# Kernel optimization log

Hardware: AMD Instinct MI355X
Metric: run time of the kernel (lower is better)

Reference implementation:

```python
import jax, jax.numpy as jnp
import numpy as np

EMBED_DIM = 256
NUM_HEADS = 8
HEAD_DIM = EMBED_DIM // NUM_HEADS
ADJ_CHANNELS = 4
B, N = 8, 1024


def setup_inputs() -> dict:
    key = jax.random.key(0)
    ks = jax.random.split(key, 12)
    s = 1.0 / np.sqrt(EMBED_DIM)
    sa = 1.0 / np.sqrt(ADJ_CHANNELS)
    return {
        "x": jax.random.normal(ks[0], (B, N, EMBED_DIM), dtype=jnp.float32),
        "adj": jax.random.uniform(ks[1], (B, N, N, ADJ_CHANNELS), dtype=jnp.float32),
        "Wq": jax.random.uniform(ks[2], (EMBED_DIM, EMBED_DIM), jnp.float32, -s, s),
        "bq": jnp.zeros((EMBED_DIM,), jnp.float32),
        "Wk": jax.random.uniform(ks[3], (EMBED_DIM, EMBED_DIM), jnp.float32, -s, s),
        "bk": jnp.zeros((EMBED_DIM,), jnp.float32),
        "Wv": jax.random.uniform(ks[4], (EMBED_DIM, EMBED_DIM), jnp.float32, -s, s),
        "bv": jnp.zeros((EMBED_DIM,), jnp.float32),
        "Wo": jax.random.uniform(ks[5], (EMBED_DIM, EMBED_DIM), jnp.float32, -s, s),
        "bo": jnp.zeros((EMBED_DIM,), jnp.float32),
        "Wa": jax.random.uniform(ks[6], (ADJ_CHANNELS, NUM_HEADS), jnp.float32, -sa, sa),
        "ba": jnp.zeros((NUM_HEADS,), jnp.float32),
    }


def reference(x, adj, Wq, bq, Wk, bk, Wv, bv, Wo, bo, Wa, ba):
    Bs, Ns, E = x.shape
    H, D = NUM_HEADS, HEAD_DIM
    def heads(W, b):
        return (x @ W + b).reshape(Bs, Ns, H, D).transpose(0, 2, 1, 3)  # [B,H,N,D]
    Q, K, V = heads(Wq, bq), heads(Wk, bk), heads(Wv, bv)
    # adjacency-derived additive bias: [B,N,N,C] -> [B,N,N,H] -> [B,H,N,N]
    bias = jnp.moveaxis(adj @ Wa + ba, -1, 1)
    scores = jnp.einsum("bhnd,bhmd->bhnm", Q, K) / np.sqrt(D) + bias
    attn = jax.nn.softmax(scores, axis=-1)
    ctx = jnp.einsum("bhnm,bhmd->bhnd", attn, V)  # [B,H,N,D]
    ctx = ctx.transpose(0, 2, 1, 3).reshape(Bs, Ns, E)
    return ctx @ Wo + bo + x
```

## Files before the change

kernel.cpp:

```cpp
#include <hip/hip_runtime.h>
#include <hip/hip_bf16.h>

#define BATCH 8
#define SEQ   1024
#define EMB   256
#define NH    8
#define HD    32
#define QSCALE 0.2550030053f

typedef __attribute__((ext_vector_type(8))) short short8;
typedef __attribute__((ext_vector_type(4))) float floatx4;

__device__ __forceinline__ ushort f2bf(float f) {
    __hip_bfloat16 h = __float2bfloat16(f);
    return *reinterpret_cast<ushort*>(&h);
}

__device__ __forceinline__ void gload_lds16(const float4* g, float4* l) {
    __builtin_amdgcn_global_load_lds(
        (const __attribute__((address_space(1))) unsigned int*)g,
        (__attribute__((address_space(3))) unsigned int*)l, 16, 0, 0);
}

__global__ __launch_bounds__(256) void prep_kernel(
    const float* __restrict__ Wq, const float* __restrict__ Wk,
    const float* __restrict__ Wv, const float* __restrict__ Wo,
    ushort* __restrict__ Wqt, ushort* __restrict__ Wkt,
    ushort* __restrict__ Wvt, ushort* __restrict__ Wot)
{
    __shared__ float tilebuf[32][33];
    const int blk = blockIdx.x;
    const int mat = blk >> 6, tile = blk & 63;
    const int ti = tile >> 3, tj = tile & 7;
    const float* W = (mat == 0) ? Wq : (mat == 1) ? Wk : (mat == 2) ? Wv : Wo;
    ushort* Wt = (mat == 0) ? Wqt : (mat == 1) ? Wkt : (mat == 2) ? Wvt : Wot;
    const float scale = (mat == 0) ? QSCALE : 1.0f;

    const int tx = threadIdx.x & 31, ty = threadIdx.x >> 5;
    #pragma unroll
    for (int p = 0; p < 4; ++p)
        tilebuf[ty + p * 8][tx] = W[(size_t)(ti * 32 + ty + p * 8) * EMB + tj * 32 + tx];
    __syncthreads();
    #pragma unroll
    for (int p = 0; p < 4; ++p)
        Wt[(size_t)(tj * 32 + ty + p * 8) * EMB + ti * 32 + tx] =
            f2bf(tilebuf[tx][ty + p * 8] * scale);
}

__global__ __launch_bounds__(256) void qkv_gemm(
    const float* __restrict__ x,
    const ushort* __restrict__ Wqt, const ushort* __restrict__ Wkt,
    const ushort* __restrict__ Wvt,
    const float* __restrict__ bq, const float* __restrict__ bk,
    const float* __restrict__ bv,
    ushort* __restrict__ Qb, ushort* __restrict__ Kb, ushort* __restrict__ Vt)
{
    const int mat = blockIdx.y;
    const ushort* __restrict__ Wt = (mat == 0) ? Wqt : (mat == 1) ? Wkt : Wvt;
    const float* __restrict__ bias = (mat == 0) ? bq : (mat == 1) ? bk : bv;
    const float bscale = (mat == 0) ? QSCALE : 1.0f;

    const int w = threadIdx.x >> 6, lane = threadIdx.x & 63;
    const int quad = lane >> 4, l16 = lane & 15;
    const int row0 = blockIdx.x * 64 + w * 16;

    floatx4 acc[16];
    #pragma unroll
    for (int i = 0; i < 16; ++i) acc[i] = (floatx4){0.f, 0.f, 0.f, 0.f};

    const float* __restrict__ xrow = x + (size_t)(row0 + l16) * EMB + quad * 8;

    #pragma unroll
    for (int ks = 0; ks < 8; ++ks) {
        const float4 xa0 = *(const float4*)(xrow + ks * 32);
        const float4 xa1 = *(const float4*)(xrow + ks * 32 + 4);
        ushort au[8] = {f2bf(xa0.x), f2bf(xa0.y), f2bf(xa0.z), f2bf(xa0.w),
                        f2bf(xa1.x), f2bf(xa1.y), f2bf(xa1.z), f2bf(xa1.w)};
        const short8 a = *(const short8*)au;
        #pragma unroll
        for (int i = 0; i < 16; ++i) {
            const short8 bf = *(const short8*)(Wt + (size_t)(i * 16 + l16) * EMB + ks * 32 + quad * 8);
            acc[i] = __builtin_amdgcn_mfma_f32_16x16x32_bf16(a, bf, acc[i], 0, 0, 0);
        }
    }

    const int gr0 = row0 + quad * 4;
    if (mat < 2) {
        ushort* __restrict__ dst = (mat == 0) ? Qb : Kb;
        #pragma unroll
        for (int i = 0; i < 16; ++i) {
            const int c = i * 16 + l16, h = c >> 5, d = c & (HD - 1);
            const float bb = bias[c] * bscale;
            #pragma unroll
            for (int r = 0; r < 4; ++r) {
                const int gr = gr0 + r, b = gr >> 10, n = gr & (SEQ - 1);
                dst[((size_t)(b * NH + h) * SEQ + n) * HD + d] = f2bf(acc[i][r] + bb);
            }
        }
    } else {
        const int b = gr0 >> 10, n0 = gr0 & (SEQ - 1);
        #pragma unroll
        for (int i = 0; i < 16; ++i) {
            const int c = i * 16 + l16, h = c >> 5, d = c & (HD - 1);
            const float bb = bias[c];
            ushort4 t4;
            t4.x = f2bf(acc[i][0] + bb); t4.y = f2bf(acc[i][1] + bb);
            t4.z = f2bf(acc[i][2] + bb); t4.w = f2bf(acc[i][3] + bb);
            *(ushort4*)(Vt + ((size_t)(b * NH + h) * HD + d) * SEQ + n0) = t4;
        }
    }
}

__global__ __launch_bounds__(512) void attn_kernel(
    const ushort* __restrict__ Qb, const ushort* __restrict__ Kb,
    const ushort* __restrict__ Vt, const float* __restrict__ adj,
    const float* __restrict__ Wa, const float* __restrict__ ba,
    float* __restrict__ cp, float* __restrict__ lsum)
{
    __shared__ float4 Atile[2][16][65];
    __shared__ ushort Plds[NH][2][16][36];
    const int tid = threadIdx.x, h = tid >> 6, lane = tid & 63;
    const int quad = lane >> 4, l16 = lane & 15;
    const int q0 = blockIdx.x * 16, b = blockIdx.y, z = blockIdx.z;
    const int bh = b * NH + h;
    const int kz = z * 512;

    const float LOG2E = 1.4426950408889634f;
    const float wa0 = Wa[0 * NH + h] * LOG2E, wa1 = Wa[1 * NH + h] * LOG2E;
    const float wa2 = Wa[2 * NH + h] * LOG2E, wa3 = Wa[3 * NH + h] * LOG2E;
    const float bah = ba[h] * LOG2E;

    const short8 aq = *(const short8*)(Qb + ((size_t)bh * SEQ + q0 + l16) * HD + quad * 8);

    floatx4 o0 = {0.f, 0.f, 0.f, 0.f}, o1 = {0.f, 0.f, 0.f, 0.f};
    float lrow[4] = {0.f, 0.f, 0.f, 0.f};

    const float4* __restrict__ adjb = (const float4*)adj + (size_t)b * SEQ * SEQ;
    const float4* __restrict__ asrc0 = adjb + (size_t)(q0 + 2 * h)     * SEQ + kz + lane;
    const float4* __restrict__ asrc1 = adjb + (size_t)(q0 + 2 * h + 1) * SEQ + kz + lane;

    const ushort* __restrict__ Kbase = Kb + (size_t)bh * SEQ * HD + (size_t)l16 * HD + quad * 8;
    const ushort* __restrict__ Vb0 = Vt + ((size_t)bh * HD + l16) * SEQ + quad * 8;
    const ushort* __restrict__ Vb1 = Vt + ((size_t)bh * HD + 16 + l16) * SEQ + quad * 8;

    gload_lds16(asrc0, &Atile[0][2 * h][0]);
    gload_lds16(asrc1, &Atile[0][2 * h + 1][0]);
    __syncthreads();

    for (int it = 0; it < 8; ++it) {
        const int cur = it & 1;
        const int key0 = kz + it * 64;

        if (it < 7) {
            gload_lds16(asrc0 + (it + 1) * 64, &Atile[cur ^ 1][2 * h][0]);
            gload_lds16(asrc1 + (it + 1) * 64, &Atile[cur ^ 1][2 * h + 1][0]);
        }

        const short8 k0 = *(const short8*)(Kbase + (size_t)(key0)      * HD);
        const short8 k1 = *(const short8*)(Kbase + (size_t)(key0 + 16) * HD);
        const short8 k2 = *(const short8*)(Kbase + (size_t)(key0 + 32) * HD);
        const short8 k3 = *(const short8*)(Kbase + (size_t)(key0 + 48) * HD);
        const floatx4 zz = {0.f, 0.f, 0.f, 0.f};
        floatx4 s0 = __builtin_amdgcn_mfma_f32_16x16x32_bf16(aq, k0, zz, 0, 0, 0);
        floatx4 s1 = __builtin_amdgcn_mfma_f32_16x16x32_bf16(aq, k1, zz, 0, 0, 0);
        floatx4 s2 = __builtin_amdgcn_mfma_f32_16x16x32_bf16(aq, k2, zz, 0, 0, 0);
        floatx4 s3 = __builtin_amdgcn_mfma_f32_16x16x32_bf16(aq, k3, zz, 0, 0, 0);

        #pragma unroll
        for (int r = 0; r < 4; ++r) {
            const int row = quad * 4 + r;
            const float4 a0 = Atile[cur][row][l16];
            const float4 a1 = Atile[cur][row][16 + l16];
            const float4 a2 = Atile[cur][row][32 + l16];
            const float4 a3 = Atile[cur][row][48 + l16];
            const float b0 = fmaf(a0.x, wa0, fmaf(a0.y, wa1, fmaf(a0.z, wa2, fmaf(a0.w, wa3, bah))));
            const float b1 = fmaf(a1.x, wa0, fmaf(a1.y, wa1, fmaf(a1.z, wa2, fmaf(a1.w, wa3, bah))));
            const float b2 = fmaf(a2.x, wa0, fmaf(a2.y, wa1, fmaf(a2.z, wa2, fmaf(a2.w, wa3, bah))));
            const float b3 = fmaf(a3.x, wa0, fmaf(a3.y, wa1, fmaf(a3.z, wa2, fmaf(a3.w, wa3, bah))));
            const float p0 = exp2f(s0[r] + b0);
            const float p1 = exp2f(s1[r] + b1);
            const float p2 = exp2f(s2[r] + b2);
            const float p3 = exp2f(s3[r] + b3);
            lrow[r] += (p0 + p1) + (p2 + p3);
            Plds[h][0][row][l16]      = f2bf(p0);
            Plds[h][0][row][16 + l16] = f2bf(p1);
            Plds[h][1][row][l16]      = f2bf(p2);
            Plds[h][1][row][16 + l16] = f2bf(p3);
        }
        __builtin_amdgcn_s_waitcnt(0xc07f);

        const short8 ap0 = *(const short8*)&Plds[h][0][l16][quad * 8];
        const short8 ap1 = *(const short8*)&Plds[h][1][l16][quad * 8];
        const short8 v0 = *(const short8*)(Vb0 + key0);
        const short8 v1 = *(const short8*)(Vb1 + key0);
        const short8 v2 = *(const short8*)(Vb0 + key0 + 32);
        const short8 v3 = *(const short8*)(Vb1 + key0 + 32);
        o0 = __builtin_amdgcn_mfma_f32_16x16x32_bf16(ap0, v0, o0, 0, 0, 0);
        o1 = __builtin_amdgcn_mfma_f32_16x16x32_bf16(ap0, v1, o1, 0, 0, 0);
        o0 = __builtin_amdgcn_mfma_f32_16x16x32_bf16(ap1, v2, o0, 0, 0, 0);
        o1 = __builtin_amdgcn_mfma_f32_16x16x32_bf16(ap1, v3, o1, 0, 0, 0);

        __syncthreads();
    }

    #pragma unroll
    for (int r = 0; r < 4; ++r) {
        lrow[r] += __shfl_xor(lrow[r], 1, 64);
        lrow[r] += __shfl_xor(lrow[r], 2, 64);
        lrow[r] += __shfl_xor(lrow[r], 4, 64);
        lrow[r] += __shfl_xor(lrow[r], 8, 64);
    }

    float* __restrict__ cpz = cp + (size_t)z * BATCH * SEQ * EMB;
    float* __restrict__ lsz = lsum + (size_t)z * BATCH * SEQ * NH;
    #pragma unroll
    for (int r = 0; r < 4; ++r) {
        const size_t grow = (size_t)b * SEQ + q0 + quad * 4 + r;
        cpz[grow * EMB + h * HD + l16]      = o0[r];
        cpz[grow * EMB + h * HD + 16 + l16] = o1[r];
        if (l16 == 0) lsz[grow * NH + h] = lrow[r];
    }
}

__global__ __launch_bounds__(256) void outproj_gemm(
    const float* __restrict__ cp, const float* __restrict__ lsum,
    const ushort* __restrict__ Wot, const float* __restrict__ bo,
    const float* __restrict__ x, float* __restrict__ out)
{
    const int w = threadIdx.x >> 6, lane = threadIdx.x & 63;
    const int quad = lane >> 4, l16 = lane & 15;
    const int row0 = blockIdx.x * 64 + w * 16;
    const int arow = row0 + l16;
    const float* __restrict__ cp1 = cp + (size_t)BATCH * SEQ * EMB;
    const float* __restrict__ l1  = lsum + (size_t)BATCH * SEQ * NH;

    floatx4 acc[16];
    #pragma unroll
    for (int i = 0; i < 16; ++i) acc[i] = (floatx4){0.f, 0.f, 0.f, 0.f};

    #pragma unroll
    for (int ks = 0; ks < 8; ++ks) {
        const float invl = 1.0f / (lsum[(size_t)arow * NH + ks] + l1[(size_t)arow * NH + ks]);
        const size_t cb = (size_t)arow * EMB + ks * 32 + quad * 8;
        const float4 c00 = *(const float4*)(cp + cb);
        const float4 c01 = *(const float4*)(cp + cb + 4);
        const float4 c10 = *(const float4*)(cp1 + cb);
        const float4 c11 = *(const float4*)(cp1 + cb + 4);
        ushort au[8] = {
            f2bf((c00.x + c10.x) * invl), f2bf((c00.y + c10.y) * invl),
            f2bf((c00.z + c10.z) * invl), f2bf((c00.w + c10.w) * invl),
            f2bf((c01.x + c11.x) * invl), f2bf((c01.y + c11.y) * invl),
            f2bf((c01.z + c11.z) * invl), f2bf((c01.w + c11.w) * invl)};
        const short8 a = *(const short8*)au;
        #pragma unroll
        for (int i = 0; i < 16; ++i) {
            const short8 bfr = *(const short8*)(Wot + (size_t)(i * 16 + l16) * EMB + ks * 32 + quad * 8);
            acc[i] = __builtin_amdgcn_mfma_f32_16x16x32_bf16(a, bfr, acc[i], 0, 0, 0);
        }
    }

    const int gr0 = row0 + quad * 4;
    #pragma unroll
    for (int i = 0; i < 16; ++i) {
        const int c = i * 16 + l16;
        const float bov = bo[c];
        #pragma unroll
        for (int r = 0; r < 4; ++r) {
            const size_t idx = (size_t)(gr0 + r) * EMB + c;
            out[idx] = acc[i][r] + bov + x[idx];
        }
    }
}

extern "C" void kernel_launch(void* const* d_in, const int* in_sizes, int n_in,
                              void* d_out, int out_size, void* d_ws, size_t ws_size,
                              hipStream_t stream) {
    const float* x   = (const float*)d_in[0];
    const float* adj = (const float*)d_in[1];
    const float* Wq  = (const float*)d_in[2];
    const float* bq  = (const float*)d_in[3];
    const float* Wk  = (const float*)d_in[4];
    const float* bk  = (const float*)d_in[5];
    const float* Wv  = (const float*)d_in[6];
    const float* bv  = (const float*)d_in[7];
    const float* Wo  = (const float*)d_in[8];
    const float* bo  = (const float*)d_in[9];
    const float* Wa  = (const float*)d_in[10];
    const float* ba  = (const float*)d_in[11];

    const size_t per = (size_t)BATCH * NH * SEQ * HD;
    ushort* Qb  = (ushort*)d_ws;
    ushort* Kb  = Qb + per;
    ushort* Vt  = Kb + per;
    ushort* Wqt = Vt + per;
    ushort* Wkt = Wqt + EMB * EMB;
    ushort* Wvt = Wkt + EMB * EMB;
    ushort* Wot = Wvt + EMB * EMB;
    float*  cp  = (float*)(Wot + EMB * EMB);
    float*  ls  = cp + 2 * (size_t)BATCH * SEQ * EMB;

    prep_kernel<<<256, 256, 0, stream>>>(Wq, Wk, Wv, Wo, Wqt, Wkt, Wvt, Wot);
    qkv_gemm<<<dim3(BATCH * SEQ / 64, 3), 256, 0, stream>>>(
        x, Wqt, Wkt, Wvt, bq, bk, bv, Qb, Kb, Vt);
    attn_kernel<<<dim3(SEQ / 16, BATCH, 2), 512, 0, stream>>>(
        Qb, Kb, Vt, adj, Wa, ba, cp, ls);
    outproj_gemm<<<BATCH * SEQ / 64, 256, 0, stream>>>(
        cp, ls, Wot, bo, x, (float*)d_out);
}
```

Measured before the change: 300.6 us.

## Compute transposed scores in attention to pass P via shuffles instead of LDS

The attention kernel now computes S^T (K as the A operand, Q as B), so each lane holds probabilities for one query row across keys. The P tile is packed to bf16 pairs and redistributed with cross-lane shuffles into the B-operand layout for the PV MFMA, removing the per-wave LDS staging buffer and its waitcnt. Row-sum reduction and output stores are adjusted to the transposed layout, and launch bounds gain a minimum-occupancy hint. It adds shuffle instructions and changes the adj LDS read pattern, which could introduce bank conflicts.

```diff
diff --git a/kernel.cpp b/kernel.cpp
--- a/kernel.cpp
+++ b/kernel.cpp
@@ -14,6 +14,9 @@
 __device__ __forceinline__ ushort f2bf(float f) {
     __hip_bfloat16 h = __float2bfloat16(f);
     return *reinterpret_cast<ushort*>(&h);
+}
+__device__ __forceinline__ unsigned int pack2bf(float lo, float hi) {
+    return (unsigned int)f2bf(lo) | ((unsigned int)f2bf(hi) << 16);
 }
 
 __device__ __forceinline__ void gload_lds16(const float4* g, float4* l) {
@@ -111,14 +114,13 @@
     }
 }
 
-__global__ __launch_bounds__(512) void attn_kernel(
+__global__ __launch_bounds__(512, 8) void attn_kernel(
     const ushort* __restrict__ Qb, const ushort* __restrict__ Kb,
     const ushort* __restrict__ Vt, const float* __restrict__ adj,
     const float* __restrict__ Wa, const float* __restrict__ ba,
     float* __restrict__ cp, float* __restrict__ lsum)
 {
     __shared__ float4 Atile[2][16][65];
-    __shared__ ushort Plds[NH][2][16][36];
     const int tid = threadIdx.x, h = tid >> 6, lane = tid & 63;
     const int quad = lane >> 4, l16 = lane & 15;
     const int q0 = blockIdx.x * 16, b = blockIdx.y, z = blockIdx.z;
@@ -133,7 +135,7 @@
     const short8 aq = *(const short8*)(Qb + ((size_t)bh * SEQ + q0 + l16) * HD + quad * 8);
 
     floatx4 o0 = {0.f, 0.f, 0.f, 0.f}, o1 = {0.f, 0.f, 0.f, 0.f};
-    float lrow[4] = {0.f, 0.f, 0.f, 0.f};
+    float lacc = 0.f;
 
     const float4* __restrict__ adjb = (const float4*)adj + (size_t)b * SEQ * SEQ;
     const float4* __restrict__ asrc0 = adjb + (size_t)(q0 + 2 * h)     * SEQ + kz + lane;
@@ -143,83 +145,83 @@
     const ushort* __restrict__ Vb0 = Vt + ((size_t)bh * HD + l16) * SEQ + quad * 8;
     const ushort* __restrict__ Vb1 = Vt + ((size_t)bh * HD + 16 + l16) * SEQ + quad * 8;
 
+    const int laneA = l16 | ((quad & 1) << 5);
+    const int laneB = laneA + 16;
+    const bool lowsel = quad < 2;
+
     gload_lds16(asrc0, &Atile[0][2 * h][0]);
     gload_lds16(asrc1, &Atile[0][2 * h + 1][0]);
     __syncthreads();
 
     for (int it = 0; it < 8; ++it) {
         const int cur = it & 1;
-        const int key0 = kz + it * 64;
-
         if (it < 7) {
             gload_lds16(asrc0 + (it + 1) * 64, &Atile[cur ^ 1][2 * h][0]);
             gload_lds16(asrc1 + (it + 1) * 64, &Atile[cur ^ 1][2 * h + 1][0]);
         }
-
-        const short8 k0 = *(const short8*)(Kbase + (size_t)(key0)      * HD);
-        const short8 k1 = *(const short8*)(Kbase + (size_t)(key0 + 16) * HD);
-        const short8 k2 = *(const short8*)(Kbase + (size_t)(key0 + 32) * HD);
-        const short8 k3 = *(const short8*)(Kbase + (size_t)(key0 + 48) * HD);
-        const floatx4 zz = {0.f, 0.f, 0.f, 0.f};
-        floatx4 s0 = __builtin_amdgcn_mfma_f32_16x16x32_bf16(aq, k0, zz, 0, 0, 0);
-        floatx4 s1 = __builtin_amdgcn_mfma_f32_16x16x32_bf16(aq, k1, zz, 0, 0, 0);
-        floatx4 s2 = __builtin_amdgcn_mfma_f32_16x16x32_bf16(aq, k2, zz, 0, 0, 0);
-        floatx4 s3 = __builtin_amdgcn_mfma_f32_16x16x32_bf16(aq, k3, zz, 0, 0, 0);
-
-        #pragma unroll
-        for (int r = 0; r < 4; ++r) {
-            const int row = quad * 4 + r;
-            const float4 a0 = Atile[cur][row][l16];
-            const float4 a1 = Atile[cur][row][16 + l16];
-            const float4 a2 = Atile[cur][row][32 + l16];
-            const float4 a3 = Atile[cur][row][48 + l16];
-            const float b0 = fmaf(a0.x, wa0, fmaf(a0.y, wa1, fmaf(a0.z, wa2, fmaf(a0.w, wa3, bah))));
-            const float b1 = fmaf(a1.x, wa0, fmaf(a1.y, wa1, fmaf(a1.z, wa2, fmaf(a1.w, wa3, bah))));
-            const float b2 = fmaf(a2.x, wa0, fmaf(a2.y, wa1, fmaf(a2.z, wa2, fmaf(a2.w, wa3, bah))));
-            const float b3 = fmaf(a3.x, wa0, fmaf(a3.y, wa1, fmaf(a3.z, wa2, fmaf(a3.w, wa3, bah))));
-            const float p0 = exp2f(s0[r] + b0);
-            const float p1 = exp2f(s1[r] + b1);
-            const float p2 = exp2f(s2[r] + b2);
-            const float p3 = exp2f(s3[r] + b3);
-            lrow[r] += (p0 + p1) + (p2 + p3);
-            Plds[h][0][row][l16]      = f2bf(p0);
-            Plds[h][0][row][16 + l16] = f2bf(p1);
-            Plds[h][1][row][l16]      = f2bf(p2);
-            Plds[h][1][row][16 + l16] = f2bf(p3);
-        }
-        __builtin_amdgcn_s_waitcnt(0xc07f);
-
-        const short8 ap0 = *(const short8*)&Plds[h][0][l16][quad * 8];
-        const short8 ap1 = *(const short8*)&Plds[h][1][l16][quad * 8];
-        const short8 v0 = *(const short8*)(Vb0 + key0);
-        const short8 v1 = *(const short8*)(Vb1 + key0);
-        const short8 v2 = *(const short8*)(Vb0 + key0 + 32);
-        const short8 v3 = *(const short8*)(Vb1 + key0 + 32);
-        o0 = __builtin_amdgcn_mfma_f32_16x16x32_bf16(ap0, v0, o0, 0, 0, 0);
-        o1 = __builtin_amdgcn_mfma_f32_16x16x32_bf16(ap0, v1, o1, 0, 0, 0);
-        o0 = __builtin_amdgcn_mfma_f32_16x16x32_bf16(ap1, v2, o0, 0, 0, 0);
-        o1 = __builtin_amdgcn_mfma_f32_16x16x32_bf16(ap1, v3, o1, 0, 0, 0);
-
+        const int key0 = kz + it * 64;
+
+        #pragma unroll
+        for (int c = 0; c < 2; ++c) {
+            const int kc = key0 + c * 32;
+            const short8 ka = *(const short8*)(Kbase + (size_t)kc * HD);
+            const short8 kb = *(const short8*)(Kbase + (size_t)(kc + 16) * HD);
+            const floatx4 zz = {0.f, 0.f, 0.f, 0.f};
+            floatx4 sA = __builtin_amdgcn_mfma_f32_16x16x32_bf16(ka, aq, zz, 0, 0, 0);
+            floatx4 sB = __builtin_amdgcn_mfma_f32_16x16x32_bf16(kb, aq, zz, 0, 0, 0);
+
+            float pA[4], pB[4];
+            #pragma unroll
+            for (int r = 0; r < 4; ++r) {
+                const int col = c * 32 + 4 * quad + r;
+                const float4 a0 = Atile[cur][l16][col];
+                const float4 a1 = Atile[cur][l16][col + 16];
+                const float b0 = fmaf(a0.x, wa0, fmaf(a0.y, wa1, fmaf(a0.z, wa2, fmaf(a0.w, wa3, bah))));
+                const float b1 = fmaf(a1.x, wa0, fmaf(a1.y, wa1, fmaf(a1.z, wa2, fmaf(a1.w, wa3, bah))));
+                pA[r] = exp2f(sA[r] + b0);
+                pB[r] = exp2f(sB[r] + b1);
+                lacc += pA[r] + pB[r];
+            }
+            const unsigned int d0 = pack2bf(pA[0], pA[1]);
+            const unsigned int d1 = pack2bf(pA[2], pA[3]);
+            const unsigned int d2 = pack2bf(pB[0], pB[1]);
+            const unsigned int d3 = pack2bf(pB[2], pB[3]);
+            const int t0A = __shfl((int)d0, laneA, 64);
+            const int t2A = __shfl((int)d2, laneA, 64);
+            const int t1A = __shfl((int)d1, laneA, 64);
+            const int t3A = __shfl((int)d3, laneA, 64);
+            const int t0B = __shfl((int)d0, laneB, 64);
+            const int t2B = __shfl((int)d2, laneB, 64);
+            const int t1B = __shfl((int)d1, laneB, 64);
+            const int t3B = __shfl((int)d3, laneB, 64);
+            int4 rr;
+            rr.x = lowsel ? t0A : t2A;
+            rr.y = lowsel ? t1A : t3A;
+            rr.z = lowsel ? t0B : t2B;
+            rr.w = lowsel ? t1B : t3B;
+            const short8 bp = __builtin_bit_cast(short8, rr);
+
+            const short8 va0 = *(const short8*)(Vb0 + kc);
+            const short8 va1 = *(const short8*)(Vb1 + kc);
+            o0 = __builtin_amdgcn_mfma_f32_16x16x32_bf16(va0, bp, o0, 0, 0, 0);
+            o1 = __builtin_amdgcn_mfma_f32_16x16x32_bf16(va1, bp, o1, 0, 0, 0);
+        }
         __syncthreads();
     }
 
-    #pragma unroll
-    for (int r = 0; r < 4; ++r) {
-        lrow[r] += __shfl_xor(lrow[r], 1, 64);
-        lrow[r] += __shfl_xor(lrow[r], 2, 64);
-        lrow[r] += __shfl_xor(lrow[r], 4, 64);
-        lrow[r] += __shfl_xor(lrow[r], 8, 64);
-    }
+    lacc += __shfl_xor(lacc, 16, 64);
+    lacc += __shfl_xor(lacc, 32, 64);
 
     float* __restrict__ cpz = cp + (size_t)z * BATCH * SEQ * EMB;
     float* __restrict__ lsz = lsum + (size_t)z * BATCH * SEQ * NH;
+    const size_t grow = (size_t)b * SEQ + q0 + l16;
     #pragma unroll
     for (int r = 0; r < 4; ++r) {
-        const size_t grow = (size_t)b * SEQ + q0 + quad * 4 + r;
-        cpz[grow * EMB + h * HD + l16]      = o0[r];
-        cpz[grow * EMB + h * HD + 16 + l16] = o1[r];
-        if (l16 == 0) lsz[grow * NH + h] = lrow[r];
-    }
+        cpz[grow * EMB + h * HD + quad * 4 + r]      = o0[r];
+        cpz[grow * EMB + h * HD + 16 + quad * 4 + r] = o1[r];
+    }
+    if (lane < 16)
+        lsz[((size_t)b * SEQ + q0 + lane) * NH + h] = lacc;
 }
 
 __global__ __launch_bounds__(256) void outproj_gemm(
```

New measurement: 313.0 us. 4.1% more time.
